# Performance work log

Measured on AMD Instinct MI355X. Metric: run time of the kernel, lower is better.

## Reference

```python
import jax, jax.numpy as jnp
import numpy as np

ALPHA = 0.5
ITERATIONS = 10
N_CLASSES = 64


def setup_inputs() -> dict:
    key = jax.random.key(0)
    k1, k2, k3, k4 = jax.random.split(key, 4)
    d_in, d_emb = 512, 256
    n_support, n_query = 4096, 4096
    support = jax.random.normal(k1, (1, n_support, d_in), dtype=jnp.float32)
    query = jax.random.normal(k2, (1, n_query, d_in), dtype=jnp.float32)
    # encoder weight, scaled like a typical init so embeddings are O(1)
    W = jax.random.normal(k3, (d_in, d_emb), dtype=jnp.float32) / np.sqrt(d_in)
    support_labels = jax.random.randint(k4, (n_support,), 0, N_CLASSES, dtype=jnp.int64)
    return {"support": support, "query": query, "W": W, "support_labels": support_labels}


def reference(support, query, W, support_labels):
    n_support = support.shape[1]
    n_query = query.shape[1]
    d_in = support.shape[-1]

    # encoder: flatten episode dim, linear projection
    support_emb = support.reshape(-1, d_in) @ W        # [n_support, d_emb]
    query_emb = query.reshape(-1, d_in) @ W            # [n_query, d_emb]
    all_emb = jnp.concatenate([support_emb, query_emb], axis=0)  # [N, d_emb]

    # similarity graph and row-normalized adjacency
    similarity = all_emb @ all_emb.T                   # [N, N]
    adjacency = (similarity > 0.5).astype(jnp.float32)
    degree = adjacency.sum(axis=1, keepdims=True)
    degree = jnp.where(degree == 0, 1.0, degree)
    normalized = adjacency / degree                    # [N, N]

    # initial label matrix: one-hot for support rows, zeros for query rows
    support_onehot = jax.nn.one_hot(support_labels, N_CLASSES, dtype=jnp.float32)
    label_init = jnp.concatenate(
        [support_onehot, jnp.zeros((n_query, N_CLASSES), dtype=jnp.float32)], axis=0
    )  # [N, C]

    def step(_, labels):
        return (1.0 - ALPHA) * labels + ALPHA * (normalized @ labels)

    labels = jax.lax.fori_loop(0, ITERATIONS, step, label_init)
    query_labels = labels[n_support:]                  # [n_query, C]
    return query_labels
```

## Files before the change

### kernel.cpp

```cpp
#include <hip/hip_runtime.h>

#define NSUP 4096
#define NTOT 8192
#define DIN  512
#define DEMB 256
#define NCLS 64

typedef __attribute__((ext_vector_type(8))) short bf16x8;
typedef __attribute__((ext_vector_type(4))) float f32x4;
typedef __attribute__((ext_vector_type(4))) unsigned int u32x4;

__device__ inline unsigned short f2bf(float x) {
  unsigned int u = __builtin_bit_cast(unsigned int, x);
  u += 0x7FFFu + ((u >> 16) & 1u);
  return (unsigned short)(u >> 16);
}
__device__ inline float bf2f(unsigned short h) {
  unsigned int u = ((unsigned int)h) << 16;
  return __builtin_bit_cast(float, u);
}

__device__ inline size_t lfrag(int i, int c) {
  return (((size_t)(i >> 5) * (NCLS / 16) + (c >> 4)) * 64 +
          (c & 15) + 16 * ((i >> 3) & 3)) * 8 + (i & 7);
}

__global__ __launch_bounds__(256) void splitX(
    const float* __restrict__ support, const float* __restrict__ query,
    unsigned short* __restrict__ XhF, unsigned short* __restrict__ XlF) {
  int w = threadIdx.x >> 6, lane = threadIdx.x & 63;
  int row = blockIdx.x * 4 + w;
  const float* X = (row < NSUP) ? (support + (size_t)row * DIN)
                                : (query + (size_t)(row - NSUP) * DIN);
  const float4* p = (const float4*)(X + lane * 8);
  float4 a = p[0], b = p[1];
  float v[8] = {a.x, a.y, a.z, a.w, b.x, b.y, b.z, b.w};
  bf16x8 hv, lv;
  #pragma unroll
  for (int j = 0; j < 8; j++) {
    unsigned short h = f2bf(v[j]);
    hv[j] = (short)h;
    lv[j] = (short)f2bf(v[j] - bf2f(h));
  }
  size_t off = (((size_t)(row >> 4) * (DIN / 32) + (lane >> 2)) * 64 +
                (row & 15) + 16 * (lane & 3)) * 8;
  *reinterpret_cast<bf16x8*>(XhF + off) = hv;
  *reinterpret_cast<bf16x8*>(XlF + off) = lv;
}

__global__ __launch_bounds__(256) void splitW(
    const float* __restrict__ W, unsigned short* __restrict__ WhF,
    unsigned short* __restrict__ WlF) {
  int idx = blockIdx.x * 256 + threadIdx.x;
  int n = idx & 255, kb8 = idx >> 8;
  bf16x8 hv, lv;
  #pragma unroll
  for (int j = 0; j < 8; j++) {
    float v = W[(size_t)(kb8 * 8 + j) * DEMB + n];
    unsigned short h = f2bf(v);
    hv[j] = (short)h;
    lv[j] = (short)f2bf(v - bf2f(h));
  }
  size_t off = (((size_t)(n >> 4) * (DIN / 32) + (kb8 >> 2)) * 64 +
                (n & 15) + 16 * (kb8 & 3)) * 8;
  *reinterpret_cast<bf16x8*>(WhF + off) = hv;
  *reinterpret_cast<bf16x8*>(WlF + off) = lv;
}

__global__ __launch_bounds__(256) void emb_mfma(
    const unsigned short* __restrict__ XhF, const unsigned short* __restrict__ XlF,
    const unsigned short* __restrict__ WhF, const unsigned short* __restrict__ WlF,
    unsigned short* __restrict__ ehiF, unsigned short* __restrict__ eloF) {
  __shared__ float lds[4][16][65];
  int lane = threadIdx.x & 63, w = threadIdx.x >> 6;
  int l15 = lane & 15, lg = lane >> 4;
  int rowblk0 = blockIdx.x * 2;
  f32x4 acc[2][4] = {};
  for (int kb = 0; kb < DIN / 32; kb++) {
    bf16x8 ah[2], al[2], bh[4], bl[4];
    #pragma unroll
    for (int fm = 0; fm < 2; fm++) {
      size_t o = (((size_t)(rowblk0 + fm) * (DIN / 32) + kb) * 64 + lane) * 8;
      ah[fm] = *reinterpret_cast<const bf16x8*>(XhF + o);
      al[fm] = *reinterpret_cast<const bf16x8*>(XlF + o);
    }
    #pragma unroll
    for (int fn = 0; fn < 4; fn++) {
      size_t o = (((size_t)(w * 4 + fn) * (DIN / 32) + kb) * 64 + lane) * 8;
      bh[fn] = *reinterpret_cast<const bf16x8*>(WhF + o);
      bl[fn] = *reinterpret_cast<const bf16x8*>(WlF + o);
    }
    #pragma unroll
    for (int fm = 0; fm < 2; fm++)
      #pragma unroll
      for (int fn = 0; fn < 4; fn++) {
        acc[fm][fn] = __builtin_amdgcn_mfma_f32_16x16x32_bf16(ah[fm], bh[fn], acc[fm][fn], 0, 0, 0);
        acc[fm][fn] = __builtin_amdgcn_mfma_f32_16x16x32_bf16(ah[fm], bl[fn], acc[fm][fn], 0, 0, 0);
        acc[fm][fn] = __builtin_amdgcn_mfma_f32_16x16x32_bf16(al[fm], bh[fn], acc[fm][fn], 0, 0, 0);
        acc[fm][fn] = __builtin_amdgcn_mfma_f32_16x16x32_bf16(al[fm], bl[fn], acc[fm][fn], 0, 0, 0);
      }
  }
  for (int fm = 0; fm < 2; fm++) {
    #pragma unroll
    for (int fn = 0; fn < 4; fn++)
      #pragma unroll
      for (int r = 0; r < 4; r++)
        lds[w][lg * 4 + r][fn * 16 + l15] = acc[fm][fn][r];
    __syncthreads();
    #pragma unroll
    for (int cb = 0; cb < 2; cb++) {
      const float* src = &lds[w][l15][cb * 32 + lg * 8];
      bf16x8 hv, lv;
      #pragma unroll
      for (int j = 0; j < 8; j++) {
        float v = src[j];
        unsigned short h = f2bf(v);
        hv[j] = (short)h;
        lv[j] = (short)f2bf(v - bf2f(h));
      }
      size_t off = (((size_t)(rowblk0 + fm) * (DEMB / 32) + w * 2 + cb) * 64 + lane) * 8;
      *reinterpret_cast<bf16x8*>(ehiF + off) = hv;
      *reinterpret_cast<bf16x8*>(eloF + off) = lv;
    }
    __syncthreads();
  }
}

__global__ __launch_bounds__(256) void sim_kernel(
    const unsigned short* __restrict__ ehiF, const unsigned short* __restrict__ eloF,
    unsigned int* __restrict__ Apk) {
  int bx = blockIdx.x, by = blockIdx.y;
  if (bx < by) return;
  __shared__ unsigned short LTn[128][8];
  __shared__ unsigned short LTt[128][8];
  int lane = threadIdx.x & 63;
  int w = threadIdx.x >> 6, wm = w >> 1, wn = w & 1;
  int l15 = lane & 15, lg = lane >> 4;
  int arb = by * 8 + wm * 4, brb = bx * 8 + wn * 4;

  f32x4 acc[4][4] = {};
  for (int kb = 0; kb < DEMB / 32; kb++) {
    bf16x8 bh[4], bl[4];
    #pragma unroll
    for (int fn = 0; fn < 4; fn++) {
      size_t o = (((size_t)(brb + fn) * (DEMB / 32) + kb) * 64 + lane) * 8;
      bh[fn] = *reinterpret_cast<const bf16x8*>(ehiF + o);
      bl[fn] = *reinterpret_cast<const bf16x8*>(eloF + o);
    }
    #pragma unroll
    for (int fm = 0; fm < 4; fm++) {
      size_t o = (((size_t)(arb + fm) * (DEMB / 32) + kb) * 64 + lane) * 8;
      bf16x8 ah = *reinterpret_cast<const bf16x8*>(ehiF + o);
      bf16x8 al = *reinterpret_cast<const bf16x8*>(eloF + o);
      #pragma unroll
      for (int fn = 0; fn < 4; fn++) {
        acc[fm][fn] = __builtin_amdgcn_mfma_f32_16x16x32_bf16(ah, bh[fn], acc[fm][fn], 0, 0, 0);
        acc[fm][fn] = __builtin_amdgcn_mfma_f32_16x16x32_bf16(ah, bl[fn], acc[fm][fn], 0, 0, 0);
        acc[fm][fn] = __builtin_amdgcn_mfma_f32_16x16x32_bf16(al, bh[fn], acc[fm][fn], 0, 0, 0);
      }
    }
  }
  #pragma unroll
  for (int fm = 0; fm < 4; fm++)
    #pragma unroll
    for (int fn = 0; fn < 4; fn++) {
      unsigned long long bal[4];
      #pragma unroll
      for (int r = 0; r < 4; r++) {
        bal[r] = __ballot(acc[fm][fn][r] > 0.5f);
        if (l15 == 0)
          LTn[wm * 64 + fm * 16 + lg * 4 + r][wn * 4 + fn] =
              (unsigned short)(bal[r] >> (lg * 16));
      }
      unsigned int tv = 0;
      #pragma unroll
      for (int p = 0; p < 16; p++) {
        unsigned int half = (unsigned int)(bal[p & 3] >> ((p >> 2) * 16));
        tv |= ((half >> l15) & 1u) << p;
      }
      if (lg == 0) LTt[wn * 64 + fn * 16 + l15][wm * 4 + fm] = (unsigned short)tv;
    }
  __syncthreads();
  #pragma unroll
  for (int pass = 0; pass < 2; pass++) {
    int idx = pass * 256 + threadIdx.x;
    int rb4 = idx >> 6, ln = idx & 63;
    int lr = rb4 * 16 + (ln & 15), Lg = ln >> 4;
    unsigned int d = 0, d2 = 0;
    #pragma unroll
    for (int t = 0; t < 4; t++) {
      int bix = t * 4 + Lg;
      unsigned int u = LTn[lr][bix >> 1];
      d |= ((u >> ((bix & 1) * 8)) & 0xffu) << (t * 8);
      unsigned int u2 = LTt[lr][bix >> 1];
      d2 |= ((u2 >> ((bix & 1) * 8)) & 0xffu) << (t * 8);
    }
    Apk[((size_t)(by * 8 + rb4) * 64 + bx) * 64 + ln] = d;
    Apk[((size_t)(bx * 8 + rb4) * 64 + by) * 64 + ln] = d2;
  }
}

__global__ __launch_bounds__(256) void degree_kernel(
    const unsigned int* __restrict__ Apk, float* __restrict__ rdeg) {
  __shared__ int dg[4][16];
  int rowblk = blockIdx.x;
  int w = threadIdx.x >> 6, lane = threadIdx.x & 63;
  const unsigned int* base = Apk + (size_t)rowblk * 4096;
  int cnt = 0;
  #pragma unroll
  for (int s = 0; s < 16; s++) cnt += __popc(base[(w * 16 + s) * 64 + lane]);
  cnt += __shfl_xor(cnt, 16);
  cnt += __shfl_xor(cnt, 32);
  if (lane < 16) dg[w][lane] = cnt;
  __syncthreads();
  if (threadIdx.x < 16) {
    int c = dg[0][threadIdx.x] + dg[1][threadIdx.x] + dg[2][threadIdx.x] + dg[3][threadIdx.x];
    rdeg[rowblk * 16 + threadIdx.x] = (c == 0) ? 1.f : 1.f / (float)c;
  }
}

__global__ __launch_bounds__(256) void init_labels(
    const int* __restrict__ slab, float* __restrict__ labels,
    unsigned short* __restrict__ LtF) {
  int idx = blockIdx.x * 256 + threadIdx.x;
  int i = idx >> 6, c = idx & 63;
  float v = 0.f;
  if (i < NSUP && slab[i] == c) v = 1.f;
  labels[idx] = v;
  LtF[lfrag(i, c)] = f2bf(v);
}

__global__ __launch_bounds__(512) void prop_kernel(
    const unsigned int* __restrict__ Apk, const unsigned short* __restrict__ LtinF,
    const float* __restrict__ rdeg, float* __restrict__ labels,
    unsigned short* __restrict__ LtoutF, float* __restrict__ outq, int last) {
  __shared__ float red[8][16][67];
  int lane = threadIdx.x & 63;
  int wk = threadIdx.x >> 6;
  int l15 = lane & 15, lg = lane >> 4;
  int rowblk = blockIdx.x;
  const unsigned int* ap = Apk + ((size_t)rowblk * 64 + wk * 8) * 64 + lane;
  f32x4 acc[4] = {};
  #pragma unroll 2
  for (int s4 = 0; s4 < 8; s4++) {
    unsigned int d = ap[s4 * 64];
    #pragma unroll
    for (int t = 0; t < 4; t++) {
      unsigned int bb = (d >> (8 * t)) & 0xffu;
      u32x4 uu;
      uu.x = ((bb & 1u)   ? 0x3F80u : 0u) | ((bb & 2u)   ? 0x3F800000u : 0u);
      uu.y = ((bb & 4u)   ? 0x3F80u : 0u) | ((bb & 8u)   ? 0x3F800000u : 0u);
      uu.z = ((bb & 16u)  ? 0x3F80u : 0u) | ((bb & 32u)  ? 0x3F800000u : 0u);
      uu.w = ((bb & 64u)  ? 0x3F80u : 0u) | ((bb & 128u) ? 0x3F800000u : 0u);
      bf16x8 a = __builtin_bit_cast(bf16x8, uu);
      int kstep = (wk * 8 + s4) * 4 + t;
      #pragma unroll
      for (int fn = 0; fn < 4; fn++) {
        bf16x8 b = *reinterpret_cast<const bf16x8*>(
            LtinF + (((size_t)kstep * 4 + fn) * 64 + lane) * 8);
        acc[fn] = __builtin_amdgcn_mfma_f32_16x16x32_bf16(a, b, acc[fn], 0, 0, 0);
      }
    }
  }
  #pragma unroll
  for (int fn = 0; fn < 4; fn++)
    #pragma unroll
    for (int r = 0; r < 4; r++)
      red[wk][lg * 4 + r][fn * 16 + l15] = acc[fn][r];
  __syncthreads();
  for (int e = threadIdx.x; e < 16 * 64; e += 512) {
    int il = e >> 6, c = e & 63;
    float s = 0.f;
    #pragma unroll
    for (int p = 0; p < 8; p++) s += red[p][il][c];
    int i = rowblk * 16 + il;
    size_t idx = (size_t)i * NCLS + c;
    float v = 0.5f * labels[idx] + 0.5f * (s * rdeg[i]);
    labels[idx] = v;
    LtoutF[lfrag(i, c)] = f2bf(v);
    if (last && i >= NSUP) outq[idx - (size_t)NSUP * NCLS] = v;
  }
}

extern "C" void kernel_launch(void* const* d_in, const int* in_sizes, int n_in,
                              void* d_out, int out_size, void* d_ws, size_t ws_size,
                              hipStream_t stream) {
  const float* support = (const float*)d_in[0];
  const float* query   = (const float*)d_in[1];
  const float* W       = (const float*)d_in[2];
  const int*   slab    = (const int*)d_in[3];
  float* out = (float*)d_out;
  char* ws = (char*)d_ws;
  const size_t MB = (size_t)1 << 20;
  unsigned short* XhF    = (unsigned short*)(ws);
  unsigned int*   Apk    = (unsigned int*)(ws);
  unsigned short* XlF    = (unsigned short*)(ws + 8 * MB);
  unsigned short* ehiF   = (unsigned short*)(ws + 16 * MB);
  unsigned short* eloF   = (unsigned short*)(ws + 20 * MB);
  unsigned short* WhF    = (unsigned short*)(ws + 24 * MB);
  unsigned short* WlF    = (unsigned short*)(ws + 24 * MB + 256 * 1024);
  float*          labels = (float*)(ws + 25 * MB);
  unsigned short* Lt0    = (unsigned short*)(ws + 27 * MB);
  unsigned short* Lt1    = (unsigned short*)(ws + 28 * MB);
  float*          rdeg   = (float*)(ws + 29 * MB);

  splitX<<<NTOT / 4, 256, 0, stream>>>(support, query, XhF, XlF);
  splitW<<<DIN * DEMB / 8 / 256, 256, 0, stream>>>(W, WhF, WlF);
  emb_mfma<<<NTOT / 32, 256, 0, stream>>>(XhF, XlF, WhF, WlF, ehiF, eloF);
  sim_kernel<<<dim3(64, 64), 256, 0, stream>>>(ehiF, eloF, Apk);
  degree_kernel<<<NTOT / 16, 256, 0, stream>>>(Apk, rdeg);
  init_labels<<<NTOT * NCLS / 256, 256, 0, stream>>>(slab, labels, Lt0);
  for (int t = 0; t < 10; t++) {
    unsigned short* Li = (t & 1) ? Lt1 : Lt0;
    unsigned short* Lo = (t & 1) ? Lt0 : Lt1;
    prop_kernel<<<NTOT / 16, 512, 0, stream>>>(Apk, Li, rdeg, labels, Lo, out, (t == 9) ? 1 : 0);
  }
}
```

Measured before the change: 391.2 us.

## Split-K propagation with bigger row tiles and triangular sim grid

The propagation kernel becomes a split-K GEMM. Each block handles 128 rows by one eighth of K and writes partial sums to a workspace buffer. The last block to arrive for each row group, found with an atomic counter, reduces the partials and applies the label update. This raises reuse of the label operand across four row blocks per wave, at the cost of extra global traffic for partials and a fence-based completion scheme. The similarity kernel now launches only upper-triangle blocks in an interleaved order, so no blocks are launched just to exit.

```diff
diff --git a/kernel.cpp b/kernel.cpp
--- a/kernel.cpp
+++ b/kernel.cpp
@@ -5,6 +5,7 @@
 #define DIN  512
 #define DEMB 256
 #define NCLS 64
+#define PKS  8
 
 typedef __attribute__((ext_vector_type(8))) short bf16x8;
 typedef __attribute__((ext_vector_type(4))) float f32x4;
@@ -129,8 +130,14 @@
 __global__ __launch_bounds__(256) void sim_kernel(
     const unsigned short* __restrict__ ehiF, const unsigned short* __restrict__ eloF,
     unsigned int* __restrict__ Apk) {
-  int bx = blockIdx.x, by = blockIdx.y;
-  if (bx < by) return;
+  int bid = (blockIdx.x & 7) * 260 + (blockIdx.x >> 3);
+  int r = 2079 - bid;
+  int j = (int)((sqrtf((float)(8 * r + 1)) - 1.0f) * 0.5f);
+  while ((j + 1) * (j + 2) / 2 <= r) ++j;
+  while (j * (j + 1) / 2 > r) --j;
+  int by = 63 - j;
+  int bx = 63 - (r - j * (j + 1) / 2);
+
   __shared__ unsigned short LTn[128][8];
   __shared__ unsigned short LTt[128][8];
   int lane = threadIdx.x & 63;
@@ -166,11 +173,11 @@
     for (int fn = 0; fn < 4; fn++) {
       unsigned long long bal[4];
       #pragma unroll
-      for (int r = 0; r < 4; r++) {
-        bal[r] = __ballot(acc[fm][fn][r] > 0.5f);
+      for (int r4 = 0; r4 < 4; r4++) {
+        bal[r4] = __ballot(acc[fm][fn][r4] > 0.5f);
         if (l15 == 0)
-          LTn[wm * 64 + fm * 16 + lg * 4 + r][wn * 4 + fn] =
-              (unsigned short)(bal[r] >> (lg * 16));
+          LTn[wm * 64 + fm * 16 + lg * 4 + r4][wn * 4 + fn] =
+              (unsigned short)(bal[r4] >> (lg * 16));
       }
       unsigned int tv = 0;
       #pragma unroll
@@ -221,8 +228,9 @@
 
 __global__ __launch_bounds__(256) void init_labels(
     const int* __restrict__ slab, float* __restrict__ labels,
-    unsigned short* __restrict__ LtF) {
+    unsigned short* __restrict__ LtF, int* __restrict__ cnt) {
   int idx = blockIdx.x * 256 + threadIdx.x;
+  if (idx < 10 * 64) cnt[idx] = 0;
   int i = idx >> 6, c = idx & 63;
   float v = 0.f;
   if (i < NSUP && slab[i] == c) v = 1.f;
@@ -230,55 +238,94 @@
   LtF[lfrag(i, c)] = f2bf(v);
 }
 
-__global__ __launch_bounds__(512) void prop_kernel(
+#define RED(k, row, col) red[k][row][(col) ^ ((((row) >> 2) & 3) << 4)]
+__global__ __launch_bounds__(512, 4) void prop_kernel(
     const unsigned int* __restrict__ Apk, const unsigned short* __restrict__ LtinF,
     const float* __restrict__ rdeg, float* __restrict__ labels,
-    unsigned short* __restrict__ LtoutF, float* __restrict__ outq, int last) {
-  __shared__ float red[8][16][67];
+    unsigned short* __restrict__ LtoutF, float* __restrict__ outq,
+    float* __restrict__ Cpart, int* __restrict__ cnt, int last) {
+  __shared__ float red[4][64][64];
   int lane = threadIdx.x & 63;
-  int wk = threadIdx.x >> 6;
+  int w = threadIdx.x >> 6;
+  int wr = w >> 2, wk = w & 3;
   int l15 = lane & 15, lg = lane >> 4;
-  int rowblk = blockIdx.x;
-  const unsigned int* ap = Apk + ((size_t)rowblk * 64 + wk * 8) * 64 + lane;
-  f32x4 acc[4] = {};
-  #pragma unroll 2
-  for (int s4 = 0; s4 < 8; s4++) {
-    unsigned int d = ap[s4 * 64];
+  int ks = blockIdx.x, rg = blockIdx.y;
+  int rb0 = rg * 8 + wr * 4;
+  int s4base = ks * 8 + wk * 2;
+
+  f32x4 acc[4][4] = {};
+  #pragma unroll
+  for (int s4 = 0; s4 < 2; s4++) {
+    unsigned int ad[4];
+    #pragma unroll
+    for (int rb = 0; rb < 4; rb++)
+      ad[rb] = Apk[((size_t)(rb0 + rb) * 64 + (s4base + s4)) * 64 + lane];
     #pragma unroll
     for (int t = 0; t < 4; t++) {
-      unsigned int bb = (d >> (8 * t)) & 0xffu;
-      u32x4 uu;
-      uu.x = ((bb & 1u)   ? 0x3F80u : 0u) | ((bb & 2u)   ? 0x3F800000u : 0u);
-      uu.y = ((bb & 4u)   ? 0x3F80u : 0u) | ((bb & 8u)   ? 0x3F800000u : 0u);
-      uu.z = ((bb & 16u)  ? 0x3F80u : 0u) | ((bb & 32u)  ? 0x3F800000u : 0u);
-      uu.w = ((bb & 64u)  ? 0x3F80u : 0u) | ((bb & 128u) ? 0x3F800000u : 0u);
-      bf16x8 a = __builtin_bit_cast(bf16x8, uu);
-      int kstep = (wk * 8 + s4) * 4 + t;
-      #pragma unroll
-      for (int fn = 0; fn < 4; fn++) {
-        bf16x8 b = *reinterpret_cast<const bf16x8*>(
+      int kstep = (s4base + s4) * 4 + t;
+      bf16x8 b[4];
+      #pragma unroll
+      for (int fn = 0; fn < 4; fn++)
+        b[fn] = *reinterpret_cast<const bf16x8*>(
             LtinF + (((size_t)kstep * 4 + fn) * 64 + lane) * 8);
-        acc[fn] = __builtin_amdgcn_mfma_f32_16x16x32_bf16(a, b, acc[fn], 0, 0, 0);
-      }
-    }
-  }
-  #pragma unroll
-  for (int fn = 0; fn < 4; fn++)
-    #pragma unroll
-    for (int r = 0; r < 4; r++)
-      red[wk][lg * 4 + r][fn * 16 + l15] = acc[fn][r];
+      #pragma unroll
+      for (int rb = 0; rb < 4; rb++) {
+        unsigned int bb = (ad[rb] >> (8 * t)) & 0xffu;
+        u32x4 uu;
+        uu.x = ((bb & 1u)   ? 0x3F80u : 0u) | ((bb & 2u)   ? 0x3F800000u : 0u);
+        uu.y = ((bb & 4u)   ? 0x3F80u : 0u) | ((bb & 8u)   ? 0x3F800000u : 0u);
+        uu.z = ((bb & 16u)  ? 0x3F80u : 0u) | ((bb & 32u)  ? 0x3F800000u : 0u);
+        uu.w = ((bb & 64u)  ? 0x3F80u : 0u) | ((bb & 128u) ? 0x3F800000u : 0u);
+        bf16x8 a = __builtin_bit_cast(bf16x8, uu);
+        #pragma unroll
+        for (int fn = 0; fn < 4; fn++)
+          acc[rb][fn] = __builtin_amdgcn_mfma_f32_16x16x32_bf16(a, b[fn], acc[rb][fn], 0, 0, 0);
+      }
+    }
+  }
+  float* cp = Cpart + (size_t)ks * (NTOT * NCLS);
+  #pragma unroll
+  for (int p = 0; p < 2; p++) {
+    #pragma unroll
+    for (int rbl = 0; rbl < 2; rbl++) {
+      int rb = p * 2 + rbl;
+      #pragma unroll
+      for (int fn = 0; fn < 4; fn++)
+        #pragma unroll
+        for (int r4 = 0; r4 < 4; r4++)
+          RED(wk, wr * 32 + rbl * 16 + lg * 4 + r4, fn * 16 + l15) = acc[rb][fn][r4];
+    }
+    __syncthreads();
+    #pragma unroll
+    for (int e = 0; e < 8; e++) {
+      int idx = e * 512 + (int)threadIdx.x;
+      int rr = idx >> 6, c = idx & 63;
+      float s = RED(0, rr, c) + RED(1, rr, c) + RED(2, rr, c) + RED(3, rr, c);
+      int grow = rg * 128 + (rr >> 5) * 64 + p * 32 + (rr & 31);
+      cp[(size_t)grow * 64 + c] = s;
+    }
+    __syncthreads();
+  }
+  int* sflag = (int*)&red[0][0][0];
+  if (threadIdx.x == 0) {
+    __threadfence();
+    *sflag = atomicAdd(&cnt[rg], 1);
+  }
   __syncthreads();
-  for (int e = threadIdx.x; e < 16 * 64; e += 512) {
-    int il = e >> 6, c = e & 63;
-    float s = 0.f;
-    #pragma unroll
-    for (int p = 0; p < 8; p++) s += red[p][il][c];
-    int i = rowblk * 16 + il;
-    size_t idx = (size_t)i * NCLS + c;
-    float v = 0.5f * labels[idx] + 0.5f * (s * rdeg[i]);
-    labels[idx] = v;
-    LtoutF[lfrag(i, c)] = f2bf(v);
-    if (last && i >= NSUP) outq[idx - (size_t)NSUP * NCLS] = v;
+  if (*sflag == PKS - 1) {
+    __threadfence();
+    for (int e = threadIdx.x; e < 128 * 64; e += 512) {
+      int il = e >> 6, c = e & 63;
+      int i = rg * 128 + il;
+      size_t idx = (size_t)i * NCLS + c;
+      float s = 0.f;
+      #pragma unroll
+      for (int k = 0; k < PKS; k++) s += Cpart[(size_t)k * NTOT * NCLS + idx];
+      float v = 0.5f * labels[idx] + 0.5f * (s * rdeg[i]);
+      labels[idx] = v;
+      LtoutF[lfrag(i, c)] = f2bf(v);
+      if (last && i >= NSUP) outq[idx - (size_t)NSUP * NCLS] = v;
+    }
   }
 }
 
@@ -295,24 +342,27 @@
   unsigned short* XhF    = (unsigned short*)(ws);
   unsigned int*   Apk    = (unsigned int*)(ws);
   unsigned short* XlF    = (unsigned short*)(ws + 8 * MB);
-  unsigned short* ehiF   = (unsigned short*)(ws + 16 * MB);
-  unsigned short* eloF   = (unsigned short*)(ws + 20 * MB);
-  unsigned short* WhF    = (unsigned short*)(ws + 24 * MB);
-  unsigned short* WlF    = (unsigned short*)(ws + 24 * MB + 256 * 1024);
-  float*          labels = (float*)(ws + 25 * MB);
-  unsigned short* Lt0    = (unsigned short*)(ws + 27 * MB);
-  unsigned short* Lt1    = (unsigned short*)(ws + 28 * MB);
-  float*          rdeg   = (float*)(ws + 29 * MB);
+  float*          Cpart  = (float*)(ws + 8 * MB);
+  unsigned short* ehiF   = (unsigned short*)(ws + 24 * MB);
+  unsigned short* eloF   = (unsigned short*)(ws + 28 * MB);
+  unsigned short* WhF    = (unsigned short*)(ws + 32 * MB);
+  unsigned short* WlF    = (unsigned short*)(ws + 32 * MB + 256 * 1024);
+  float*          labels = (float*)(ws + 33 * MB);
+  unsigned short* Lt0    = (unsigned short*)(ws + 35 * MB);
+  unsigned short* Lt1    = (unsigned short*)(ws + 36 * MB);
+  float*          rdeg   = (float*)(ws + 37 * MB);
+  int*            cnt    = (int*)(ws + 37 * MB + 64 * 1024);
 
   splitX<<<NTOT / 4, 256, 0, stream>>>(support, query, XhF, XlF);
   splitW<<<DIN * DEMB / 8 / 256, 256, 0, stream>>>(W, WhF, WlF);
   emb_mfma<<<NTOT / 32, 256, 0, stream>>>(XhF, XlF, WhF, WlF, ehiF, eloF);
-  sim_kernel<<<dim3(64, 64), 256, 0, stream>>>(ehiF, eloF, Apk);
+  sim_kernel<<<2080, 256, 0, stream>>>(ehiF, eloF, Apk);
   degree_kernel<<<NTOT / 16, 256, 0, stream>>>(Apk, rdeg);
-  init_labels<<<NTOT * NCLS / 256, 256, 0, stream>>>(slab, labels, Lt0);
+  init_labels<<<NTOT * NCLS / 256, 256, 0, stream>>>(slab, labels, Lt0, cnt);
   for (int t = 0; t < 10; t++) {
     unsigned short* Li = (t & 1) ? Lt1 : Lt0;
     unsigned short* Lo = (t & 1) ? Lt0 : Lt1;
-    prop_kernel<<<NTOT / 16, 512, 0, stream>>>(Apk, Li, rdeg, labels, Lo, out, (t == 9) ? 1 : 0);
-  }
-}
+    prop_kernel<<<dim3(PKS, 64), 512, 0, stream>>>(Apk, Li, rdeg, labels, Lo, out,
+                                                   Cpart, cnt + t * 64, (t == 9) ? 1 : 0);
+  }
+}
```

New measurement: 1.297 ms. 232% more time.
